# Kernel optimization log

Hardware: AMD Instinct MI355X
Metric: run time of the kernel (lower is better)

## Reference

```python
import jax, jax.numpy as jnp
import numpy as np

N_LEVELS = 16  # 2**4, bit = 4 in QuantLinear


def _sum_to(g, shape):
    # reduce grad g to broadcast shape `shape`
    extra = g.ndim - len(shape)
    if extra:
        g = g.sum(axis=tuple(range(extra)))
    axes = tuple(i for i, (gs, s) in enumerate(zip(g.shape, shape)) if s == 1 and gs != 1)
    if axes:
        g = g.sum(axis=axes, keepdims=True)
    return g.reshape(shape)


@jax.custom_vjp
def ste_round(x):
    return jnp.round(x)

def _r_fwd(x):
    return jnp.round(x), None

def _r_bwd(_, g):
    return (g,)

ste_round.defvjp(_r_fwd, _r_bwd)


@jax.custom_vjp
def dclip(x, lo, hi):
    return jnp.clip(x, lo, hi)

def _c_fwd(x, lo, hi):
    return jnp.clip(x, lo, hi), (x, lo, hi)

def _c_bwd(res, g):
    x, lo, hi = res
    gx = jnp.where((x < lo) | (x > hi), 0.0, g)
    glo = _sum_to(jnp.where(x > lo, 0.0, g), lo.shape)
    ghi = _sum_to(jnp.where(x < hi, 0.0, g), hi.shape)
    return gx, glo, ghi

dclip.defvjp(_c_fwd, _c_bwd)


def fake_quant(x, lb, ub):
    # UniformQuantizer.forward
    delta = (ub - lb) / (N_LEVELS - 1)
    x_cut = dclip(x, lb, ub)
    x_int = ste_round((x_cut - lb) / delta)
    return x_int * delta + lb


def setup_inputs() -> dict:
    key = jax.random.key(0)
    k0, k1, k2 = jax.random.split(key, 3)
    B, S, Din, Dout = 4, 4096, 1024, 3072
    x = jax.random.normal(k0, (B, S, Din), jnp.float32)
    weight = jax.random.normal(k1, (Dout, Din), jnp.float32) * 0.02
    bias = jax.random.normal(k2, (Dout,), jnp.float32) * 0.01
    # calibrated per-tensor activation bounds, per-output-channel weight bounds
    in_lb = jnp.full((1,), -2.5, jnp.float32)
    in_ub = jnp.full((1,), 2.5, jnp.float32)
    w_ub = jnp.max(jnp.abs(weight), axis=1, keepdims=True)  # (Dout, 1)
    w_lb = -w_ub
    return {"x": x, "weight": weight, "bias": bias,
            "in_lb": in_lb, "in_ub": in_ub, "w_lb": w_lb, "w_ub": w_ub}


def reference(x, weight, bias, in_lb, in_ub, w_lb, w_ub):
    qx = fake_quant(x, in_lb, in_ub)        # [B,S,Din]
    qw = fake_quant(weight, w_lb, w_ub)     # [Dout,Din]
    return jnp.einsum('bsi,oi->bso', qx, qw) + bias
```

## Files before the change

kernel.cpp:

```cpp
#include <hip/hip_runtime.h>

typedef int i32x4 __attribute__((ext_vector_type(4)));
typedef unsigned char u8x8 __attribute__((ext_vector_type(8)));


__global__ __launch_bounds__(512) void quant_x_i8(
    const float* __restrict__ x, unsigned char* __restrict__ qx,
    float* __restrict__ Sx, const float* __restrict__ lbp,
    const float* __restrict__ ubp) {
  const float lb = lbp[0], ub = ubp[0];
  const float delta = (ub - lb) / 15.0f;
  const int tid = threadIdx.x;
  const int row_in_blk = tid >> 7;
  const int row = blockIdx.x * 4 + row_in_blk;
  const size_t base = (size_t)row * 1024 + (tid & 127) * 8;

  const float4* p = reinterpret_cast<const float4*>(x + base);
  float4 v0 = p[0], v1 = p[1];
  int k[8];
  float vv[8] = {v0.x, v0.y, v0.z, v0.w, v1.x, v1.y, v1.z, v1.w};
  int s = 0;
  u8x8 o;
#pragma unroll
  for (int j = 0; j < 8; ++j) {
    float t = fminf(fmaxf(vv[j], lb), ub);
    k[j] = (int)rintf((t - lb) / delta);
    s += k[j];
    o[j] = (unsigned char)k[j];
  }
  *reinterpret_cast<u8x8*>(qx + base) = o;

#pragma unroll
  for (int d = 32; d > 0; d >>= 1) s += __shfl_down(s, d);
  __shared__ int wsum[8];
  if ((tid & 63) == 0) wsum[tid >> 6] = s;
  __syncthreads();
  if (tid < 4) Sx[blockIdx.x * 4 + tid] = (float)(wsum[2 * tid] + wsum[2 * tid + 1]);
}

__global__ __launch_bounds__(512) void quant_w_i8(
    const float* __restrict__ w, unsigned char* __restrict__ qw,
    float* __restrict__ Sw, const float* __restrict__ lbp,
    const float* __restrict__ ubp) {
  const int tid = threadIdx.x;
  const int row_in_blk = tid >> 7;
  const int row = blockIdx.x * 4 + row_in_blk;
  const float lb = lbp[row], ub = ubp[row];
  const float delta = (ub - lb) / 15.0f;
  const size_t base = (size_t)row * 1024 + (tid & 127) * 8;

  const float4* p = reinterpret_cast<const float4*>(w + base);
  float4 v0 = p[0], v1 = p[1];
  float vv[8] = {v0.x, v0.y, v0.z, v0.w, v1.x, v1.y, v1.z, v1.w};
  int s = 0;
  u8x8 o;
#pragma unroll
  for (int j = 0; j < 8; ++j) {
    float t = fminf(fmaxf(vv[j], lb), ub);
    int k = (int)rintf((t - lb) / delta);
    s += k;
    o[j] = (unsigned char)k;
  }
  *reinterpret_cast<u8x8*>(qw + base) = o;

#pragma unroll
  for (int d = 32; d > 0; d >>= 1) s += __shfl_down(s, d);
  __shared__ int wsum[8];
  if ((tid & 63) == 0) wsum[tid >> 6] = s;
  __syncthreads();
  if (tid < 4) Sw[blockIdx.x * 4 + tid] = (float)(wsum[2 * tid] + wsum[2 * tid + 1]);
}


__device__ __forceinline__ void gload_lds16(const unsigned char* g, unsigned char* l) {
  __builtin_amdgcn_global_load_lds(
      (const __attribute__((address_space(1))) unsigned int*)g,
      (__attribute__((address_space(3))) unsigned int*)l, 16, 0, 0);
}

#define SWZ(o) ((o) ^ ((((o) >> 7) & 3) << 4))

__global__ __launch_bounds__(512, 4) void gemm_i8_kernel(
    const unsigned char* __restrict__ A, const unsigned char* __restrict__ B,
    const float* __restrict__ bias, const float* __restrict__ Sx,
    const float* __restrict__ Sw, const float* __restrict__ wlb,
    const float* __restrict__ wub, const float* __restrict__ xlb,
    const float* __restrict__ xub, float* __restrict__ C, int M, int N) {
  const int K = 1024;
  const int NKT = 16;
  __shared__ unsigned char lds[3][24576];

  const int tid = threadIdx.x;
  const int w = tid >> 6, l = tid & 63;
  const int wm = w >> 1, wn = w & 1;

  int bid = blockIdx.x;
  { const int cpx = gridDim.x >> 3; bid = (bid & 7) * cpx + (bid >> 3); }
  const int ntn = N >> 7;
  const int tm = bid / ntn, tn = bid % ntn;

  const unsigned char* gA = A + (size_t)tm * 256 * K;
  const unsigned char* gB = B + (size_t)tn * 128 * K;

  const int p0 = tid * 16, p1 = 8192 + tid * 16, pB = tid * 16;
  const int o0 = SWZ(p0), o1 = SWZ(p1), oB = SWZ(pB);
  const unsigned char* sA0 = gA + (size_t)(o0 >> 6) * K + (o0 & 63);
  const unsigned char* sA1 = gA + (size_t)(o1 >> 6) * K + (o1 & 63);
  const unsigned char* sB0 = gB + (size_t)(oB >> 6) * K + (oB & 63);

  const int lroff = (l & 15) * 64 + (((l >> 4) * 16) ^ (((l >> 1) & 3) << 4));

#define STAGE(SB, KOFF) do {                                             \
    unsigned char* Rb_ = &lds[SB][0];                                    \
    gload_lds16(sA0 + (KOFF), Rb_ + p0);                                 \
    gload_lds16(sA1 + (KOFF), Rb_ + p1);                                 \
    gload_lds16(sB0 + (KOFF), Rb_ + 16384 + pB);                         \
  } while (0)

#define RD_A(RB, F)  (*(const i32x4*)(&lds[RB][0]     + wm * 4096 + (F) * 1024 + lroff))
#define RD_B(RB, NN) (*(const i32x4*)(&lds[RB][16384] + wn * 4096 + (NN) * 1024 + lroff))

#define BAR __builtin_amdgcn_s_barrier()
#define LGKM0 do { asm volatile("s_waitcnt lgkmcnt(0)" ::: "memory");    \
                   __builtin_amdgcn_sched_barrier(0); } while (0)
#define VMC3 asm volatile("s_waitcnt vmcnt(3)" ::: "memory")

  i32x4 acc[4][4] = {};
  i32x4 av[4], bv[4];

  STAGE(0, 0);
  STAGE(1, 64);
  VMC3; BAR;

#pragma unroll
  for (int t = 0; t < NKT; ++t) {
    const int rb = t % 3, sb = (t + 2) % 3;
    const int koff = (t + 2 < NKT ? (t + 2) : 0) << 6;
#pragma unroll
    for (int f = 0; f < 4; ++f) av[f] = RD_A(rb, f);
#pragma unroll
    for (int nn = 0; nn < 4; ++nn) bv[nn] = RD_B(rb, nn);
    STAGE(sb, koff);
    VMC3;
    BAR; LGKM0;
    __builtin_amdgcn_s_setprio(1);
#pragma unroll
    for (int mm = 0; mm < 4; ++mm)
#pragma unroll
      for (int nn = 0; nn < 4; ++nn)
        acc[mm][nn] = __builtin_amdgcn_mfma_i32_16x16x64_i8(
            av[mm], bv[nn], acc[mm][nn], 0, 0, 0);
    __builtin_amdgcn_s_setprio(0);
    BAR;
  }

  const float lbx = xlb[0];
  const float dx = (xub[0] - lbx) / 15.0f;
  const int rq = (l >> 4) * 4;
  const int cn = l & 15;
  const int mb = tm * 256 + wm * 64;
  const int nb = tn * 128 + wn * 64;

  float sxr[4][4];
#pragma unroll
  for (int m = 0; m < 4; ++m) {
    const int r0 = mb + m * 16 + rq;
#pragma unroll
    for (int j = 0; j < 4; ++j) sxr[m][j] = Sx[r0 + j];
  }
#pragma unroll
  for (int n = 0; n < 4; ++n) {
    const int col = nb + n * 16 + cn;
    const float wl = wlb[col], wu = wub[col];
    const float dw = (wu - wl) / 15.0f;
    const float c1 = dx * dw;
    const float c2 = dx * wl;
    const float c3 = lbx * dw * Sw[col] + 1024.0f * lbx * wl + bias[col];
#pragma unroll
    for (int m = 0; m < 4; ++m) {
      float* cp = C + (size_t)(mb + m * 16 + rq) * N + col;
      cp[0]             = c1 * (float)acc[m][n][0] + c2 * sxr[m][0] + c3;
      cp[(size_t)N]     = c1 * (float)acc[m][n][1] + c2 * sxr[m][1] + c3;
      cp[(size_t)2 * N] = c1 * (float)acc[m][n][2] + c2 * sxr[m][2] + c3;
      cp[(size_t)3 * N] = c1 * (float)acc[m][n][3] + c2 * sxr[m][3] + c3;
    }
  }
#undef STAGE
#undef RD_A
#undef RD_B
#undef BAR
#undef LGKM0
#undef VMC3
}

extern "C" void kernel_launch(void* const* d_in, const int* in_sizes, int n_in,
                              void* d_out, int out_size, void* d_ws, size_t ws_size,
                              hipStream_t stream) {
  const float* x     = (const float*)d_in[0];
  const float* wgt   = (const float*)d_in[1];
  const float* bias  = (const float*)d_in[2];
  const float* in_lb = (const float*)d_in[3];
  const float* in_ub = (const float*)d_in[4];
  const float* w_lb  = (const float*)d_in[5];
  const float* w_ub  = (const float*)d_in[6];

  const int Dout = in_sizes[2];
  const int Din  = in_sizes[1] / Dout;
  const int M    = in_sizes[0] / Din;

  unsigned char* qx = (unsigned char*)d_ws;
  unsigned char* qw = qx + (size_t)M * Din;
  float* Sx = (float*)(qw + (size_t)Dout * Din);
  float* Sw = Sx + M;

  quant_x_i8<<<M / 4, 512, 0, stream>>>(x, qx, Sx, in_lb, in_ub);
  quant_w_i8<<<Dout / 4, 512, 0, stream>>>(wgt, qw, Sw, w_lb, w_ub);

  dim3 grid((M / 256) * (Dout / 128));
  gemm_i8_kernel<<<grid, 512, 0, stream>>>(qx, qw, bias, Sx, Sw, w_lb, w_ub,
                                           in_lb, in_ub, (float*)d_out, M, Dout);
}
```

Baseline: 99.31 us.

## Shrink GEMM tile to 128x128 with 256 threads and move vmcnt wait after MFMA

The int8 GEMM block tile drops from 256x128 with 512 threads to 128x128 with 256 threads. The grid doubles and LDS per block falls to 48KB across the three stages. The vmcnt wait for the prefetched stage now sits after the MFMA block instead of before it, so global loads overlap more with compute. Smaller tiles reuse each loaded byte less, which raises L2/HBM traffic but gives more blocks for load balancing. The quant kernels get only cosmetic cleanup.

```diff
diff --git a/kernel.cpp b/kernel.cpp
--- a/kernel.cpp
+++ b/kernel.cpp
@@ -11,22 +11,20 @@
   const float lb = lbp[0], ub = ubp[0];
   const float delta = (ub - lb) / 15.0f;
   const int tid = threadIdx.x;
-  const int row_in_blk = tid >> 7;
-  const int row = blockIdx.x * 4 + row_in_blk;
+  const int row = blockIdx.x * 4 + (tid >> 7);
   const size_t base = (size_t)row * 1024 + (tid & 127) * 8;
 
   const float4* p = reinterpret_cast<const float4*>(x + base);
   float4 v0 = p[0], v1 = p[1];
-  int k[8];
   float vv[8] = {v0.x, v0.y, v0.z, v0.w, v1.x, v1.y, v1.z, v1.w};
   int s = 0;
   u8x8 o;
 #pragma unroll
   for (int j = 0; j < 8; ++j) {
     float t = fminf(fmaxf(vv[j], lb), ub);
-    k[j] = (int)rintf((t - lb) / delta);
-    s += k[j];
-    o[j] = (unsigned char)k[j];
+    int k = (int)rintf((t - lb) / delta);
+    s += k;
+    o[j] = (unsigned char)k;
   }
   *reinterpret_cast<u8x8*>(qx + base) = o;
 
@@ -43,8 +41,7 @@
     float* __restrict__ Sw, const float* __restrict__ lbp,
     const float* __restrict__ ubp) {
   const int tid = threadIdx.x;
-  const int row_in_blk = tid >> 7;
-  const int row = blockIdx.x * 4 + row_in_blk;
+  const int row = blockIdx.x * 4 + (tid >> 7);
   const float lb = lbp[row], ub = ubp[row];
   const float delta = (ub - lb) / 15.0f;
   const size_t base = (size_t)row * 1024 + (tid & 127) * 8;
@@ -80,7 +77,7 @@
 
 #define SWZ(o) ((o) ^ ((((o) >> 7) & 3) << 4))
 
-__global__ __launch_bounds__(512, 4) void gemm_i8_kernel(
+__global__ __launch_bounds__(256, 3) void gemm_i8_kernel(
     const unsigned char* __restrict__ A, const unsigned char* __restrict__ B,
     const float* __restrict__ bias, const float* __restrict__ Sx,
     const float* __restrict__ Sw, const float* __restrict__ wlb,
@@ -88,7 +85,7 @@
     const float* __restrict__ xub, float* __restrict__ C, int M, int N) {
   const int K = 1024;
   const int NKT = 16;
-  __shared__ unsigned char lds[3][24576];
+  __shared__ unsigned char lds[3][16384];
 
   const int tid = threadIdx.x;
   const int w = tid >> 6, l = tid & 63;
@@ -99,14 +96,15 @@
   const int ntn = N >> 7;
   const int tm = bid / ntn, tn = bid % ntn;
 
-  const unsigned char* gA = A + (size_t)tm * 256 * K;
+  const unsigned char* gA = A + (size_t)tm * 128 * K;
   const unsigned char* gB = B + (size_t)tn * 128 * K;
 
-  const int p0 = tid * 16, p1 = 8192 + tid * 16, pB = tid * 16;
-  const int o0 = SWZ(p0), o1 = SWZ(p1), oB = SWZ(pB);
+  const int p0 = tid * 16, p1 = 4096 + tid * 16;
+  const int o0 = SWZ(p0), o1 = SWZ(p1);
   const unsigned char* sA0 = gA + (size_t)(o0 >> 6) * K + (o0 & 63);
   const unsigned char* sA1 = gA + (size_t)(o1 >> 6) * K + (o1 & 63);
-  const unsigned char* sB0 = gB + (size_t)(oB >> 6) * K + (oB & 63);
+  const unsigned char* sB0 = gB + (size_t)(o0 >> 6) * K + (o0 & 63);
+  const unsigned char* sB1 = gB + (size_t)(o1 >> 6) * K + (o1 & 63);
 
   const int lroff = (l & 15) * 64 + (((l >> 4) * 16) ^ (((l >> 1) & 3) << 4));
 
@@ -114,23 +112,24 @@
     unsigned char* Rb_ = &lds[SB][0];                                    \
     gload_lds16(sA0 + (KOFF), Rb_ + p0);                                 \
     gload_lds16(sA1 + (KOFF), Rb_ + p1);                                 \
-    gload_lds16(sB0 + (KOFF), Rb_ + 16384 + pB);                         \
+    gload_lds16(sB0 + (KOFF), Rb_ + 8192 + p0);                          \
+    gload_lds16(sB1 + (KOFF), Rb_ + 8192 + p1);                          \
   } while (0)
 
-#define RD_A(RB, F)  (*(const i32x4*)(&lds[RB][0]     + wm * 4096 + (F) * 1024 + lroff))
-#define RD_B(RB, NN) (*(const i32x4*)(&lds[RB][16384] + wn * 4096 + (NN) * 1024 + lroff))
+#define RD_A(RB, F)  (*(const i32x4*)(&lds[RB][0]    + wm * 4096 + (F) * 1024 + lroff))
+#define RD_B(RB, NN) (*(const i32x4*)(&lds[RB][8192] + wn * 4096 + (NN) * 1024 + lroff))
 
 #define BAR __builtin_amdgcn_s_barrier()
 #define LGKM0 do { asm volatile("s_waitcnt lgkmcnt(0)" ::: "memory");    \
                    __builtin_amdgcn_sched_barrier(0); } while (0)
-#define VMC3 asm volatile("s_waitcnt vmcnt(3)" ::: "memory")
+#define VMC4 asm volatile("s_waitcnt vmcnt(4)" ::: "memory")
 
   i32x4 acc[4][4] = {};
   i32x4 av[4], bv[4];
 
   STAGE(0, 0);
   STAGE(1, 64);
-  VMC3; BAR;
+  VMC4; BAR;
 
 #pragma unroll
   for (int t = 0; t < NKT; ++t) {
@@ -141,7 +140,6 @@
 #pragma unroll
     for (int nn = 0; nn < 4; ++nn) bv[nn] = RD_B(rb, nn);
     STAGE(sb, koff);
-    VMC3;
     BAR; LGKM0;
     __builtin_amdgcn_s_setprio(1);
 #pragma unroll
@@ -151,6 +149,7 @@
         acc[mm][nn] = __builtin_amdgcn_mfma_i32_16x16x64_i8(
             av[mm], bv[nn], acc[mm][nn], 0, 0, 0);
     __builtin_amdgcn_s_setprio(0);
+    VMC4;
     BAR;
   }
 
@@ -158,7 +157,7 @@
   const float dx = (xub[0] - lbx) / 15.0f;
   const int rq = (l >> 4) * 4;
   const int cn = l & 15;
-  const int mb = tm * 256 + wm * 64;
+  const int mb = tm * 128 + wm * 64;
   const int nb = tn * 128 + wn * 64;
 
   float sxr[4][4];
@@ -185,12 +184,13 @@
       cp[(size_t)3 * N] = c1 * (float)acc[m][n][3] + c2 * sxr[m][3] + c3;
     }
   }
+  asm volatile("s_waitcnt vmcnt(0)" ::: "memory");
 #undef STAGE
 #undef RD_A
 #undef RD_B
 #undef BAR
 #undef LGKM0
-#undef VMC3
+#undef VMC4
 }
 
 extern "C" void kernel_launch(void* const* d_in, const int* in_sizes, int n_in,
@@ -216,7 +216,7 @@
   quant_x_i8<<<M / 4, 512, 0, stream>>>(x, qx, Sx, in_lb, in_ub);
   quant_w_i8<<<Dout / 4, 512, 0, stream>>>(wgt, qw, Sw, w_lb, w_ub);
 
-  dim3 grid((M / 256) * (Dout / 128));
-  gemm_i8_kernel<<<grid, 512, 0, stream>>>(qx, qw, bias, Sx, Sw, w_lb, w_ub,
+  dim3 grid((M / 128) * (Dout / 128));
+  gemm_i8_kernel<<<grid, 256, 0, stream>>>(qx, qw, bias, Sx, Sw, w_lb, w_ub,
                                            in_lb, in_ub, (float*)d_out, M, Dout);
 }
```

New measurement: 108.0 us. 8.8% more time.
